# Performance work log

Hardware: AMD Instinct MI355X
Metric: run time of the kernel (lower is better)

Reference implementation:

```python
import jax, jax.numpy as jnp
import numpy as np

N = 1024
H = 128
W = 128
SH_DEG = 3
K = (SH_DEG + 1) ** 2  # 16

C0 = 0.28209479177387814
C1 = 0.4886025119029199
C2 = (1.0925484305920792, -1.0925484305920792, 0.31539156525252005, -1.0925484305920792, 0.5462742152960396)
C3 = (-0.5900435899266435, 2.890611442640554, -0.4570457994644658, 0.3731763325901154, -0.4570457994644658, 1.445305721320277, -0.5900435899266435)


def setup_inputs() -> dict:
    key = jax.random.key(0)
    ks = jax.random.split(key, 8)
    xy = jax.random.uniform(ks[0], (N, 2), minval=-2.0, maxval=2.0)
    z = jax.random.uniform(ks[1], (N, 1), minval=2.0, maxval=8.0)
    means3D = jnp.concatenate([xy, z], axis=1)
    sh = jax.random.normal(ks[2], (N, K, 3)) * 0.3
    opacities = jax.random.uniform(ks[3], (N,), minval=0.1, maxval=1.0)
    scales = jax.random.uniform(ks[4], (N, 3), minval=0.02, maxval=0.15)
    rotations = jax.random.normal(ks[5], (N, 4))
    cam_pos = jnp.zeros((3,), jnp.float32)
    cam_rot = jnp.eye(3, dtype=jnp.float32)  # world-to-camera rotation
    tan_half_fov = jnp.array([0.7], jnp.float32)
    bg_color = jax.random.uniform(ks[6], (3,))
    near_far = jnp.array([0.2, 100.0], jnp.float32)
    return dict(means3D=means3D, sh=sh, opacities=opacities, scales=scales,
                rotations=rotations, cam_pos=cam_pos, cam_rot=cam_rot,
                tan_half_fov=tan_half_fov, bg_color=bg_color, near_far=near_far,
                image_h=H, image_w=W, sh_degree=SH_DEG)


def _eval_sh(sh, dirs):
    # degree-3 real spherical harmonics, as in the 3DGS CUDA rasterizer
    x, y, z = dirs[:, 0:1], dirs[:, 1:2], dirs[:, 2:3]
    res = C0 * sh[:, 0]
    res = res - C1 * y * sh[:, 1] + C1 * z * sh[:, 2] - C1 * x * sh[:, 3]
    xx, yy, zz = x * x, y * y, z * z
    xy, yz, xz = x * y, y * z, x * z
    res = (res + C2[0] * xy * sh[:, 4] + C2[1] * yz * sh[:, 5]
           + C2[2] * (2.0 * zz - xx - yy) * sh[:, 6]
           + C2[3] * xz * sh[:, 7] + C2[4] * (xx - yy) * sh[:, 8])
    res = (res + C3[0] * y * (3.0 * xx - yy) * sh[:, 9]
           + C3[1] * xy * z * sh[:, 10]
           + C3[2] * y * (4.0 * zz - xx - yy) * sh[:, 11]
           + C3[3] * z * (2.0 * zz - 3.0 * xx - 3.0 * yy) * sh[:, 12]
           + C3[4] * x * (4.0 * zz - xx - yy) * sh[:, 13]
           + C3[5] * z * (xx - yy) * sh[:, 14]
           + C3[6] * x * (xx - 3.0 * yy) * sh[:, 15])
    return jnp.maximum(res + 0.5, 0.0)


def _quat_to_rot(q):
    q = q / jnp.linalg.norm(q, axis=1, keepdims=True)
    r, x, y, z = q[:, 0], q[:, 1], q[:, 2], q[:, 3]
    R = jnp.stack([
        1 - 2 * (y * y + z * z), 2 * (x * y - r * z), 2 * (x * z + r * y),
        2 * (x * y + r * z), 1 - 2 * (x * x + z * z), 2 * (y * z - r * x),
        2 * (x * z - r * y), 2 * (y * z + r * x), 1 - 2 * (x * x + y * y)],
        axis=1).reshape(-1, 3, 3)
    return R


def _forward(means3D, sh, opacities, scales, rotations, cam_pos, cam_rot,
             tan_half_fov, bg_color, near_far, image_h, image_w):
    thf = tan_half_fov[0]
    fx = image_w / (2.0 * thf)
    fy = image_h / (2.0 * thf)
    # view-space positions
    t = jnp.einsum('ij,nj->ni', cam_rot, means3D - cam_pos)  # [N,3]
    tz = t[:, 2]
    lim = 1.3 * thf
    tx = jnp.clip(t[:, 0] / tz, -lim, lim) * tz
    ty = jnp.clip(t[:, 1] / tz, -lim, lim) * tz
    # 3D covariance from quaternion + scale: Sigma = (R S)(R S)^T
    Rq = _quat_to_rot(rotations)
    M = Rq * scales[:, None, :]
    cov3 = jnp.einsum('nij,nkj->nik', M, M)
    # EWA splatting: 2D covariance via projection Jacobian
    z2 = tz * tz
    zeros = jnp.zeros_like(tz)
    J = jnp.stack([
        jnp.stack([fx / tz, zeros, -fx * tx / z2], axis=1),
        jnp.stack([zeros, fy / tz, -fy * ty / z2], axis=1)], axis=1)  # [N,2,3]
    T = jnp.einsum('nij,jk->nik', J, cam_rot)
    cov2 = jnp.einsum('nij,njk,nlk->nil', T, cov3, T)  # [N,2,2]
    a = cov2[:, 0, 0] + 0.3  # low-pass filter on diagonal (as in 3DGS)
    c = cov2[:, 1, 1] + 0.3
    b = cov2[:, 0, 1]
    det = a * c - b * b
    inv_det = 1.0 / det
    conA, conB, conC = c * inv_det, -b * inv_det, a * inv_det
    # 2D means in pixel coordinates
    mx = fx * t[:, 0] / tz + (image_w - 1.0) / 2.0
    my = fy * t[:, 1] / tz + (image_h - 1.0) / 2.0
    # view-dependent color from SH
    dirs = means3D - cam_pos
    dirs = dirs / jnp.linalg.norm(dirs, axis=1, keepdims=True)
    colors = _eval_sh(sh, dirs)  # [N,3]
    # per-pixel gaussian alpha [N, P]
    pxs = jnp.arange(image_w, dtype=jnp.float32)
    pys = jnp.arange(image_h, dtype=jnp.float32)
    gy, gx = jnp.meshgrid(pys, pxs, indexing='ij')
    px = gx.reshape(-1)
    py = gy.reshape(-1)
    dx = px[None, :] - mx[:, None]
    dy = py[None, :] - my[:, None]
    power = -0.5 * (conA[:, None] * dx * dx + conC[:, None] * dy * dy) - conB[:, None] * dx * dy
    alpha = jnp.minimum(opacities[:, None] * jnp.exp(power), 0.99)
    valid = (tz > near_far[0]) & (tz < near_far[1]) & (det > 0.0)
    alpha = jnp.where(valid[:, None] & (power <= 0.0) & (alpha >= 1.0 / 255.0), alpha, 0.0)
    # global depth sort + front-to-back alpha compositing
    order = jnp.argsort(tz)
    alpha_s = alpha[order]
    colors_s = colors[order]
    trans = jnp.cumprod(1.0 - alpha_s, axis=0)  # inclusive transmittance [N,P]
    trans_excl = jnp.concatenate([jnp.ones((1, alpha_s.shape[1]), alpha_s.dtype), trans[:-1]], axis=0)
    wgt = alpha_s * trans_excl  # blending weights
    img = jnp.einsum('np,nc->pc', wgt, colors_s) + trans[-1][:, None] * bg_color[None, :]
    return img.reshape(image_h, image_w, 3).transpose(2, 0, 1)  # [3,H,W]


def reference(means3D, sh, opacities, scales, rotations, cam_pos, cam_rot,
              tan_half_fov, bg_color, near_far, image_h, image_w, sh_degree):
    # sh_degree is fixed to 3 via the SH table size (K=16); kept for signature parity
    return _forward(means3D, sh, opacities, scales, rotations, cam_pos, cam_rot,
                    tan_half_fov, bg_color, near_far, image_h, image_w)
```

## Files before the change

### kernel.cpp

```cpp
#include <hip/hip_runtime.h>

#define NG   1024
#define IMH  128
#define IMW  128
#define NPIX (IMH * IMW)
#define SEGS 16

__global__ __launch_bounds__(256) void k_prep(
    const float* __restrict__ means,
    const float* __restrict__ sh,
    const float* __restrict__ opac,
    const float* __restrict__ scales,
    const float* __restrict__ rots,
    const float* __restrict__ campos,
    const float* __restrict__ camrot,
    const float* __restrict__ thf_p,
    const float* __restrict__ nearfar,
    float4* __restrict__ g0, float4* __restrict__ g1, float4* __restrict__ g2)
{
    __shared__ unsigned long long lk[NG];
    __shared__ int prank[16][16];

    int t = threadIdx.x;
    int b = blockIdx.x;

    float thf = thf_p[0];
    float R[9];
    #pragma unroll
    for (int k = 0; k < 9; k++) R[k] = camrot[k];
    float cp0 = campos[0], cp1 = campos[1], cp2 = campos[2];
    float near_ = nearfar[0], far_ = nearfar[1];

    #pragma unroll
    for (int j = 0; j < 4; j++) {
        int g = j * 256 + t;
        float dx = means[3 * g + 0] - cp0;
        float dy = means[3 * g + 1] - cp1;
        float dz = means[3 * g + 2] - cp2;
        float tzk = R[6] * dx + R[7] * dy + R[8] * dz;
        unsigned u = __float_as_uint(tzk);
        u = (u & 0x80000000u) ? ~u : (u | 0x80000000u);
        lk[g] = ((unsigned long long)u << 32) | (unsigned)g;
    }
    __syncthreads();

    int gl    = t & 15;
    int chunk = t >> 4;
    unsigned long long ki = lk[b * 16 + gl];
    int cnt = 0;
    int j0 = chunk * 64;
    #pragma unroll 8
    for (int j = 0; j < 64; j++) cnt += (lk[j0 + j] < ki) ? 1 : 0;
    prank[chunk][gl] = cnt;
    __syncthreads();

    if (t < 16) {
        int i = b * 16 + t;
        float fx = IMW / (2.0f * thf);
        float fy = IMH / (2.0f * thf);

        int r = 0;
        #pragma unroll
        for (int c2i = 0; c2i < 16; c2i++) r += prank[c2i][t];

        float d0x = means[3 * i + 0] - cp0;
        float d0y = means[3 * i + 1] - cp1;
        float d0z = means[3 * i + 2] - cp2;

        float tx0 = R[0] * d0x + R[1] * d0y + R[2] * d0z;
        float ty0 = R[3] * d0x + R[4] * d0y + R[5] * d0z;
        float tz  = R[6] * d0x + R[7] * d0y + R[8] * d0z;

        float lim  = 1.3f * thf;
        float invz = 1.0f / tz;
        float txc  = fminf(fmaxf(tx0 * invz, -lim), lim) * tz;
        float tyc  = fminf(fmaxf(ty0 * invz, -lim), lim) * tz;

        float4 q = ((const float4*)rots)[i];
        float qr = q.x, qx = q.y, qy = q.z, qz = q.w;
        float qn = rsqrtf(qr * qr + qx * qx + qy * qy + qz * qz);
        qr *= qn; qx *= qn; qy *= qn; qz *= qn;
        float Rq0 = 1.0f - 2.0f * (qy * qy + qz * qz);
        float Rq1 = 2.0f * (qx * qy - qr * qz);
        float Rq2 = 2.0f * (qx * qz + qr * qy);
        float Rq3 = 2.0f * (qx * qy + qr * qz);
        float Rq4 = 1.0f - 2.0f * (qx * qx + qz * qz);
        float Rq5 = 2.0f * (qy * qz - qr * qx);
        float Rq6 = 2.0f * (qx * qz - qr * qy);
        float Rq7 = 2.0f * (qy * qz + qr * qx);
        float Rq8 = 1.0f - 2.0f * (qx * qx + qy * qy);

        float sx = scales[3 * i + 0], sy = scales[3 * i + 1], sz = scales[3 * i + 2];
        float M0 = Rq0 * sx, M1 = Rq1 * sy, M2 = Rq2 * sz;
        float M3 = Rq3 * sx, M4 = Rq4 * sy, M5 = Rq5 * sz;
        float M6 = Rq6 * sx, M7 = Rq7 * sy, M8 = Rq8 * sz;

        float c00 = M0 * M0 + M1 * M1 + M2 * M2;
        float c01 = M0 * M3 + M1 * M4 + M2 * M5;
        float c02 = M0 * M6 + M1 * M7 + M2 * M8;
        float c11 = M3 * M3 + M4 * M4 + M5 * M5;
        float c12 = M3 * M6 + M4 * M7 + M5 * M8;
        float c22 = M6 * M6 + M7 * M7 + M8 * M8;

        float z2  = tz * tz;
        float J00 = fx * invz, J02 = -fx * txc / z2;
        float J11 = fy * invz, J12 = -fy * tyc / z2;

        float T00 = J00 * R[0] + J02 * R[6];
        float T01 = J00 * R[1] + J02 * R[7];
        float T02 = J00 * R[2] + J02 * R[8];
        float T10 = J11 * R[3] + J12 * R[6];
        float T11 = J11 * R[4] + J12 * R[7];
        float T12 = J11 * R[5] + J12 * R[8];

        float v00 = T00 * c00 + T01 * c01 + T02 * c02;
        float v01 = T00 * c01 + T01 * c11 + T02 * c12;
        float v02 = T00 * c02 + T01 * c12 + T02 * c22;
        float v10 = T10 * c00 + T11 * c01 + T12 * c02;
        float v11 = T10 * c01 + T11 * c11 + T12 * c12;
        float v12 = T10 * c02 + T11 * c12 + T12 * c22;

        float a  = v00 * T00 + v01 * T01 + v02 * T02 + 0.3f;
        float bb = v00 * T10 + v01 * T11 + v02 * T12;
        float c  = v10 * T10 + v11 * T11 + v12 * T12 + 0.3f;

        float det    = a * c - bb * bb;
        float invdet = 1.0f / det;
        float conA = c * invdet, conB = -bb * invdet, conC = a * invdet;

        float mx = fx * tx0 * invz + (IMW - 1) * 0.5f;
        float my = fy * ty0 * invz + (IMH - 1) * 0.5f;

        float dn = rsqrtf(d0x * d0x + d0y * d0y + d0z * d0z);
        float x = d0x * dn, y = d0y * dn, z = d0z * dn;
        float xx = x * x, yy = y * y, zz = z * z;
        float xy = x * y, yz = y * z, xz = x * z;

        float basis[16];
        basis[0]  = 0.28209479177387814f;
        basis[1]  = -0.4886025119029199f * y;
        basis[2]  =  0.4886025119029199f * z;
        basis[3]  = -0.4886025119029199f * x;
        basis[4]  =  1.0925484305920792f * xy;
        basis[5]  = -1.0925484305920792f * yz;
        basis[6]  =  0.31539156525252005f * (2.0f * zz - xx - yy);
        basis[7]  = -1.0925484305920792f * xz;
        basis[8]  =  0.5462742152960396f * (xx - yy);
        basis[9]  = -0.5900435899266435f * y * (3.0f * xx - yy);
        basis[10] =  2.890611442640554f * xy * z;
        basis[11] = -0.4570457994644658f * y * (4.0f * zz - xx - yy);
        basis[12] =  0.3731763325901154f * z * (2.0f * zz - 3.0f * xx - 3.0f * yy);
        basis[13] = -0.4570457994644658f * x * (4.0f * zz - xx - yy);
        basis[14] =  1.445305721320277f * z * (xx - yy);
        basis[15] = -0.5900435899266435f * x * (xx - 3.0f * yy);

        float f[48];
        {
            const float4* sh4 = (const float4*)(sh + i * 48);
            float4* fv = (float4*)f;
            #pragma unroll
            for (int j = 0; j < 12; j++) fv[j] = sh4[j];
        }
        float colr = 0.0f, colg = 0.0f, colb = 0.0f;
        #pragma unroll
        for (int k = 0; k < 16; k++) {
            float bk = basis[k];
            colr = fmaf(bk, f[3 * k + 0], colr);
            colg = fmaf(bk, f[3 * k + 1], colg);
            colb = fmaf(bk, f[3 * k + 2], colb);
        }
        colr = fmaxf(colr + 0.5f, 0.0f);
        colg = fmaxf(colg + 0.5f, 0.0f);
        colb = fmaxf(colb + 0.5f, 0.0f);

        bool valid = (tz > near_) && (tz < far_) && (det > 0.0f);
        float op = valid ? opac[i] : 0.0f;

        float rx, ry;
        if (op >= (1.0f / 255.0f)) {
            float s2 = 2.0f * logf(255.0f * op);
            rx = sqrtf(s2 * a) + 1e-3f;
            ry = sqrtf(s2 * c) + 1e-3f;
        } else {
            rx = -1.0f; ry = -1.0f;
        }

        g0[r] = make_float4(mx, my, rx, ry);
        g1[r] = make_float4(-0.5f * conA, -conB, -0.5f * conC, op);
        g2[r] = make_float4(colr, colg, colb, 0.0f);
    }
}

__global__ __launch_bounds__(1024) void k_comp(
    const float4* __restrict__ g0, const float4* __restrict__ g1,
    const float4* __restrict__ g2, const float* __restrict__ bg,
    float* __restrict__ out)
{
    __shared__ float4 lA[NG];
    __shared__ float4 lB[NG];
    __shared__ float  lC[NG];
    __shared__ float4 red[SEGS * 64];
    __shared__ int wcnt[16];

    int t    = threadIdx.x;
    int wid  = t >> 6;
    int lane = t & 63;
    int bx = blockIdx.x & 15, by = blockIdx.x >> 4;
    float x0 = (float)(bx * 8), y0 = (float)(by * 8);

    float4 c0 = g0[t];
    float4 c1 = g1[t];
    float4 c2 = g2[t];
    bool surv = (c0.z >= 0.0f) &&
                (c0.x + c0.z >= x0) && (c0.x - c0.z <= x0 + 7.0f) &&
                (c0.y + c0.w >= y0) && (c0.y - c0.w <= y0 + 7.0f);
    unsigned long long m = __ballot(surv);
    if (lane == 0) wcnt[wid] = __popcll(m);
    __syncthreads();

    int pre = 0, M = 0;
    #pragma unroll
    for (int w = 0; w < 16; w++) {
        int cw = wcnt[w];
        M += cw;
        if (w < wid) pre += cw;
    }
    if (surv) {
        int pos = pre + __popcll(m & ((1ull << lane) - 1ull));
        lA[pos] = make_float4(c0.x, c0.y, c1.x, c1.y);
        lB[pos] = make_float4(c1.z, c1.w, c2.x, c2.y);
        lC[pos] = c2.z;
    }
    __syncthreads();

    M = __builtin_amdgcn_readfirstlane(M);
    int len = (M + SEGS - 1) / SEGS;
    int seg = __builtin_amdgcn_readfirstlane(wid);
    int ks  = seg * len;
    int ke  = min(M, ks + len);

    float fpx = x0 + (float)(lane & 7);
    float fpy = y0 + (float)(lane >> 3);

    float T = 1.0f, cr = 0.0f, cg = 0.0f, cb = 0.0f;
    for (int k = ks; k < ke; k++) {
        float4 qA = lA[k];
        float4 qB = lB[k];
        float  qc = lC[k];
        float dx = fpx - qA.x;
        float dy = fpy - qA.y;
        float pw = fmaf(dx, fmaf(qA.z, dx, qA.w * dy), qB.x * (dy * dy));
        float al = qB.y * __expf(pw);
        al = fminf(al, 0.99f);
        bool ok = (pw <= 0.0f) && (al >= (1.0f / 255.0f));
        al = ok ? al : 0.0f;
        float w = al * T;
        cr = fmaf(w, qB.z, cr);
        cg = fmaf(w, qB.w, cg);
        cb = fmaf(w, qc, cb);
        T = fmaf(-al, T, T);
    }

    red[seg * 64 + lane] = make_float4(cr, cg, cb, T);
    __syncthreads();

    if (t < 64) {
        float Tt = 1.0f, r = 0.0f, g = 0.0f, b = 0.0f;
        #pragma unroll
        for (int s = 0; s < SEGS; s++) {
            float4 v = red[s * 64 + t];
            r = fmaf(Tt, v.x, r);
            g = fmaf(Tt, v.y, g);
            b = fmaf(Tt, v.z, b);
            Tt *= v.w;
        }
        int pix = (by * 8 + (t >> 3)) * IMW + bx * 8 + (t & 7);
        out[0 * NPIX + pix] = r + Tt * bg[0];
        out[1 * NPIX + pix] = g + Tt * bg[1];
        out[2 * NPIX + pix] = b + Tt * bg[2];
    }
}

extern "C" void kernel_launch(void* const* d_in, const int* in_sizes, int n_in,
                              void* d_out, int out_size, void* d_ws, size_t ws_size,
                              hipStream_t stream)
{
    (void)in_sizes; (void)n_in; (void)out_size; (void)ws_size;

    const float* means   = (const float*)d_in[0];
    const float* sh      = (const float*)d_in[1];
    const float* opac    = (const float*)d_in[2];
    const float* scales  = (const float*)d_in[3];
    const float* rots    = (const float*)d_in[4];
    const float* campos  = (const float*)d_in[5];
    const float* camrot  = (const float*)d_in[6];
    const float* thf     = (const float*)d_in[7];
    const float* bg      = (const float*)d_in[8];
    const float* nearfar = (const float*)d_in[9];

    char* ws = (char*)d_ws;
    float4* g0 = (float4*)(ws + 0);
    float4* g1 = (float4*)(ws + 16384);
    float4* g2 = (float4*)(ws + 32768);

    k_prep<<<64, 256, 0, stream>>>(means, sh, opac, scales, rots, campos,
                                   camrot, thf, nearfar, g0, g1, g2);
    k_comp<<<256, 1024, 0, stream>>>(g0, g1, g2, bg, (float*)d_out);
}
```

Before: 85.53 us.

## Fuse preprocessing into compositing kernel with per-tile culling and local depth sort

```diff
diff --git a/kernel.cpp b/kernel.cpp
--- a/kernel.cpp
+++ b/kernel.cpp
@@ -6,7 +6,7 @@
 #define NPIX (IMH * IMW)
 #define SEGS 16
 
-__global__ __launch_bounds__(256) void k_prep(
+__global__ __launch_bounds__(1024) void k_fused(
     const float* __restrict__ means,
     const float* __restrict__ sh,
     const float* __restrict__ opac,
@@ -16,123 +16,147 @@
     const float* __restrict__ camrot,
     const float* __restrict__ thf_p,
     const float* __restrict__ nearfar,
-    float4* __restrict__ g0, float4* __restrict__ g1, float4* __restrict__ g2)
+    const float* __restrict__ bg,
+    float* __restrict__ out)
 {
-    __shared__ unsigned long long lk[NG];
-    __shared__ int prank[16][16];
-
-    int t = threadIdx.x;
-    int b = blockIdx.x;
+    __shared__ float4 uA[NG];
+    __shared__ float2 uB[NG];
+    __shared__ unsigned long long ukey[NG];
+    __shared__ float4 lA[NG];
+    __shared__ float4 lB[NG];
+    __shared__ float  lC[NG];
+    __shared__ float4 red[SEGS * 64];
+    __shared__ int wcnt[16];
+
+    int t    = threadIdx.x;
+    int wid  = t >> 6;
+    int lane = t & 63;
+    int bx = blockIdx.x & 15, by = blockIdx.x >> 4;
+    float x0 = (float)(bx * 8), y0 = (float)(by * 8);
 
     float thf = thf_p[0];
+    float fx = IMW / (2.0f * thf);
+    float fy = IMH / (2.0f * thf);
     float R[9];
     #pragma unroll
     for (int k = 0; k < 9; k++) R[k] = camrot[k];
     float cp0 = campos[0], cp1 = campos[1], cp2 = campos[2];
     float near_ = nearfar[0], far_ = nearfar[1];
 
+    float d0x = means[3 * t + 0] - cp0;
+    float d0y = means[3 * t + 1] - cp1;
+    float d0z = means[3 * t + 2] - cp2;
+
+    float tx0 = R[0] * d0x + R[1] * d0y + R[2] * d0z;
+    float ty0 = R[3] * d0x + R[4] * d0y + R[5] * d0z;
+    float tz  = R[6] * d0x + R[7] * d0y + R[8] * d0z;
+
+    float lim  = 1.3f * thf;
+    float invz = 1.0f / tz;
+    float txc  = fminf(fmaxf(tx0 * invz, -lim), lim) * tz;
+    float tyc  = fminf(fmaxf(ty0 * invz, -lim), lim) * tz;
+
+    float4 q = ((const float4*)rots)[t];
+    float qr = q.x, qx = q.y, qy = q.z, qz = q.w;
+    float qn = rsqrtf(qr * qr + qx * qx + qy * qy + qz * qz);
+    qr *= qn; qx *= qn; qy *= qn; qz *= qn;
+    float Rq0 = 1.0f - 2.0f * (qy * qy + qz * qz);
+    float Rq1 = 2.0f * (qx * qy - qr * qz);
+    float Rq2 = 2.0f * (qx * qz + qr * qy);
+    float Rq3 = 2.0f * (qx * qy + qr * qz);
+    float Rq4 = 1.0f - 2.0f * (qx * qx + qz * qz);
+    float Rq5 = 2.0f * (qy * qz - qr * qx);
+    float Rq6 = 2.0f * (qx * qz - qr * qy);
+    float Rq7 = 2.0f * (qy * qz + qr * qx);
+    float Rq8 = 1.0f - 2.0f * (qx * qx + qy * qy);
+
+    float sx = scales[3 * t + 0], sy = scales[3 * t + 1], sz = scales[3 * t + 2];
+    float M0 = Rq0 * sx, M1 = Rq1 * sy, M2 = Rq2 * sz;
+    float M3 = Rq3 * sx, M4 = Rq4 * sy, M5 = Rq5 * sz;
+    float M6 = Rq6 * sx, M7 = Rq7 * sy, M8 = Rq8 * sz;
+
+    float c00 = M0 * M0 + M1 * M1 + M2 * M2;
+    float c01 = M0 * M3 + M1 * M4 + M2 * M5;
+    float c02 = M0 * M6 + M1 * M7 + M2 * M8;
+    float c11 = M3 * M3 + M4 * M4 + M5 * M5;
+    float c12 = M3 * M6 + M4 * M7 + M5 * M8;
+    float c22 = M6 * M6 + M7 * M7 + M8 * M8;
+
+    float z2  = tz * tz;
+    float J00 = fx * invz, J02 = -fx * txc / z2;
+    float J11 = fy * invz, J12 = -fy * tyc / z2;
+
+    float T00 = J00 * R[0] + J02 * R[6];
+    float T01 = J00 * R[1] + J02 * R[7];
+    float T02 = J00 * R[2] + J02 * R[8];
+    float T10 = J11 * R[3] + J12 * R[6];
+    float T11 = J11 * R[4] + J12 * R[7];
+    float T12 = J11 * R[5] + J12 * R[8];
+
+    float v00 = T00 * c00 + T01 * c01 + T02 * c02;
+    float v01 = T00 * c01 + T01 * c11 + T02 * c12;
+    float v02 = T00 * c02 + T01 * c12 + T02 * c22;
+    float v10 = T10 * c00 + T11 * c01 + T12 * c02;
+    float v11 = T10 * c01 + T11 * c11 + T12 * c12;
+    float v12 = T10 * c02 + T11 * c12 + T12 * c22;
+
+    float a  = v00 * T00 + v01 * T01 + v02 * T02 + 0.3f;
+    float bb = v00 * T10 + v01 * T11 + v02 * T12;
+    float c  = v10 * T10 + v11 * T11 + v12 * T12 + 0.3f;
+
+    float det    = a * c - bb * bb;
+    float invdet = 1.0f / det;
+    float conA = c * invdet, conB = -bb * invdet, conC = a * invdet;
+
+    float mx = fx * tx0 * invz + (IMW - 1) * 0.5f;
+    float my = fy * ty0 * invz + (IMH - 1) * 0.5f;
+
+    bool valid = (tz > near_) && (tz < far_) && (det > 0.0f);
+    float op = valid ? opac[t] : 0.0f;
+
+    float rx = -1.0f, ry = -1.0f;
+    if (op >= (1.0f / 255.0f)) {
+        float s2 = 2.0f * logf(255.0f * op);
+        rx = sqrtf(s2 * a) + 1e-3f;
+        ry = sqrtf(s2 * c) + 1e-3f;
+    }
+
+    bool surv = (rx >= 0.0f) &&
+                (mx + rx >= x0) && (mx - rx <= x0 + 7.0f) &&
+                (my + ry >= y0) && (my - ry <= y0 + 7.0f);
+    unsigned long long m = __ballot(surv);
+    if (lane == 0) wcnt[wid] = __popcll(m);
+    __syncthreads();
+
+    int pre = 0, M = 0;
     #pragma unroll
-    for (int j = 0; j < 4; j++) {
-        int g = j * 256 + t;
-        float dx = means[3 * g + 0] - cp0;
-        float dy = means[3 * g + 1] - cp1;
-        float dz = means[3 * g + 2] - cp2;
-        float tzk = R[6] * dx + R[7] * dy + R[8] * dz;
-        unsigned u = __float_as_uint(tzk);
+    for (int w = 0; w < 16; w++) {
+        int cw = wcnt[w];
+        M += cw;
+        if (w < wid) pre += cw;
+    }
+    if (surv) {
+        int pos = pre + __popcll(m & ((1ull << lane) - 1ull));
+        uA[pos] = make_float4(mx, my, -0.5f * conA, -conB);
+        uB[pos] = make_float2(-0.5f * conC, op);
+        unsigned u = __float_as_uint(tz);
         u = (u & 0x80000000u) ? ~u : (u | 0x80000000u);
-        lk[g] = ((unsigned long long)u << 32) | (unsigned)g;
-    }
-    __syncthreads();
-
-    int gl    = t & 15;
-    int chunk = t >> 4;
-    unsigned long long ki = lk[b * 16 + gl];
-    int cnt = 0;
-    int j0 = chunk * 64;
-    #pragma unroll 8
-    for (int j = 0; j < 64; j++) cnt += (lk[j0 + j] < ki) ? 1 : 0;
-    prank[chunk][gl] = cnt;
-    __syncthreads();
-
-    if (t < 16) {
-        int i = b * 16 + t;
-        float fx = IMW / (2.0f * thf);
-        float fy = IMH / (2.0f * thf);
-
+        ukey[pos] = ((unsigned long long)u << 32) | (unsigned)t;
+    }
+    __syncthreads();
+
+    if (t < M) {
+        unsigned long long kt = ukey[t];
         int r = 0;
-        #pragma unroll
-        for (int c2i = 0; c2i < 16; c2i++) r += prank[c2i][t];
-
-        float d0x = means[3 * i + 0] - cp0;
-        float d0y = means[3 * i + 1] - cp1;
-        float d0z = means[3 * i + 2] - cp2;
-
-        float tx0 = R[0] * d0x + R[1] * d0y + R[2] * d0z;
-        float ty0 = R[3] * d0x + R[4] * d0y + R[5] * d0z;
-        float tz  = R[6] * d0x + R[7] * d0y + R[8] * d0z;
-
-        float lim  = 1.3f * thf;
-        float invz = 1.0f / tz;
-        float txc  = fminf(fmaxf(tx0 * invz, -lim), lim) * tz;
-        float tyc  = fminf(fmaxf(ty0 * invz, -lim), lim) * tz;
-
-        float4 q = ((const float4*)rots)[i];
-        float qr = q.x, qx = q.y, qy = q.z, qz = q.w;
-        float qn = rsqrtf(qr * qr + qx * qx + qy * qy + qz * qz);
-        qr *= qn; qx *= qn; qy *= qn; qz *= qn;
-        float Rq0 = 1.0f - 2.0f * (qy * qy + qz * qz);
-        float Rq1 = 2.0f * (qx * qy - qr * qz);
-        float Rq2 = 2.0f * (qx * qz + qr * qy);
-        float Rq3 = 2.0f * (qx * qy + qr * qz);
-        float Rq4 = 1.0f - 2.0f * (qx * qx + qz * qz);
-        float Rq5 = 2.0f * (qy * qz - qr * qx);
-        float Rq6 = 2.0f * (qx * qz - qr * qy);
-        float Rq7 = 2.0f * (qy * qz + qr * qx);
-        float Rq8 = 1.0f - 2.0f * (qx * qx + qy * qy);
-
-        float sx = scales[3 * i + 0], sy = scales[3 * i + 1], sz = scales[3 * i + 2];
-        float M0 = Rq0 * sx, M1 = Rq1 * sy, M2 = Rq2 * sz;
-        float M3 = Rq3 * sx, M4 = Rq4 * sy, M5 = Rq5 * sz;
-        float M6 = Rq6 * sx, M7 = Rq7 * sy, M8 = Rq8 * sz;
-
-        float c00 = M0 * M0 + M1 * M1 + M2 * M2;
-        float c01 = M0 * M3 + M1 * M4 + M2 * M5;
-        float c02 = M0 * M6 + M1 * M7 + M2 * M8;
-        float c11 = M3 * M3 + M4 * M4 + M5 * M5;
-        float c12 = M3 * M6 + M4 * M7 + M5 * M8;
-        float c22 = M6 * M6 + M7 * M7 + M8 * M8;
-
-        float z2  = tz * tz;
-        float J00 = fx * invz, J02 = -fx * txc / z2;
-        float J11 = fy * invz, J12 = -fy * tyc / z2;
-
-        float T00 = J00 * R[0] + J02 * R[6];
-        float T01 = J00 * R[1] + J02 * R[7];
-        float T02 = J00 * R[2] + J02 * R[8];
-        float T10 = J11 * R[3] + J12 * R[6];
-        float T11 = J11 * R[4] + J12 * R[7];
-        float T12 = J11 * R[5] + J12 * R[8];
-
-        float v00 = T00 * c00 + T01 * c01 + T02 * c02;
-        float v01 = T00 * c01 + T01 * c11 + T02 * c12;
-        float v02 = T00 * c02 + T01 * c12 + T02 * c22;
-        float v10 = T10 * c00 + T11 * c01 + T12 * c02;
-        float v11 = T10 * c01 + T11 * c11 + T12 * c12;
-        float v12 = T10 * c02 + T11 * c12 + T12 * c22;
-
-        float a  = v00 * T00 + v01 * T01 + v02 * T02 + 0.3f;
-        float bb = v00 * T10 + v01 * T11 + v02 * T12;
-        float c  = v10 * T10 + v11 * T11 + v12 * T12 + 0.3f;
-
-        float det    = a * c - bb * bb;
-        float invdet = 1.0f / det;
-        float conA = c * invdet, conB = -bb * invdet, conC = a * invdet;
-
-        float mx = fx * tx0 * invz + (IMW - 1) * 0.5f;
-        float my = fy * ty0 * invz + (IMH - 1) * 0.5f;
-
-        float dn = rsqrtf(d0x * d0x + d0y * d0y + d0z * d0z);
-        float x = d0x * dn, y = d0y * dn, z = d0z * dn;
+        for (int j = 0; j < M; j++) r += (ukey[j] < kt) ? 1 : 0;
+
+        int idx = (int)(kt & 0xffffffffu);
+
+        float gx = means[3 * idx + 0] - cp0;
+        float gy = means[3 * idx + 1] - cp1;
+        float gz = means[3 * idx + 2] - cp2;
+        float dn = rsqrtf(gx * gx + gy * gy + gz * gz);
+        float x = gx * dn, y = gy * dn, z = gz * dn;
         float xx = x * x, yy = y * y, zz = z * z;
         float xy = x * y, yz = y * z, xz = x * z;
 
@@ -156,7 +180,7 @@
 
         float f[48];
         {
-            const float4* sh4 = (const float4*)(sh + i * 48);
+            const float4* sh4 = (const float4*)(sh + idx * 48);
             float4* fv = (float4*)f;
             #pragma unroll
             for (int j = 0; j < 12; j++) fv[j] = sh4[j];
@@ -173,67 +197,14 @@
         colg = fmaxf(colg + 0.5f, 0.0f);
         colb = fmaxf(colb + 0.5f, 0.0f);
 
-        bool valid = (tz > near_) && (tz < far_) && (det > 0.0f);
-        float op = valid ? opac[i] : 0.0f;
-
-        float rx, ry;
-        if (op >= (1.0f / 255.0f)) {
-            float s2 = 2.0f * logf(255.0f * op);
-            rx = sqrtf(s2 * a) + 1e-3f;
-            ry = sqrtf(s2 * c) + 1e-3f;
-        } else {
-            rx = -1.0f; ry = -1.0f;
-        }
-
-        g0[r] = make_float4(mx, my, rx, ry);
-        g1[r] = make_float4(-0.5f * conA, -conB, -0.5f * conC, op);
-        g2[r] = make_float4(colr, colg, colb, 0.0f);
-    }
-}
-
-__global__ __launch_bounds__(1024) void k_comp(
-    const float4* __restrict__ g0, const float4* __restrict__ g1,
-    const float4* __restrict__ g2, const float* __restrict__ bg,
-    float* __restrict__ out)
-{
-    __shared__ float4 lA[NG];
-    __shared__ float4 lB[NG];
-    __shared__ float  lC[NG];
-    __shared__ float4 red[SEGS * 64];
-    __shared__ int wcnt[16];
-
-    int t    = threadIdx.x;
-    int wid  = t >> 6;
-    int lane = t & 63;
-    int bx = blockIdx.x & 15, by = blockIdx.x >> 4;
-    float x0 = (float)(bx * 8), y0 = (float)(by * 8);
-
-    float4 c0 = g0[t];
-    float4 c1 = g1[t];
-    float4 c2 = g2[t];
-    bool surv = (c0.z >= 0.0f) &&
-                (c0.x + c0.z >= x0) && (c0.x - c0.z <= x0 + 7.0f) &&
-                (c0.y + c0.w >= y0) && (c0.y - c0.w <= y0 + 7.0f);
-    unsigned long long m = __ballot(surv);
-    if (lane == 0) wcnt[wid] = __popcll(m);
-    __syncthreads();
-
-    int pre = 0, M = 0;
-    #pragma unroll
-    for (int w = 0; w < 16; w++) {
-        int cw = wcnt[w];
-        M += cw;
-        if (w < wid) pre += cw;
-    }
-    if (surv) {
-        int pos = pre + __popcll(m & ((1ull << lane) - 1ull));
-        lA[pos] = make_float4(c0.x, c0.y, c1.x, c1.y);
-        lB[pos] = make_float4(c1.z, c1.w, c2.x, c2.y);
-        lC[pos] = c2.z;
-    }
-    __syncthreads();
-
-    M = __builtin_amdgcn_readfirstlane(M);
+        float4 ua = uA[t];
+        float2 ub = uB[t];
+        lA[r] = ua;
+        lB[r] = make_float4(ub.x, ub.y, colr, colg);
+        lC[r] = colb;
+    }
+    __syncthreads();
+
     int len = (M + SEGS - 1) / SEGS;
     int seg = __builtin_amdgcn_readfirstlane(wid);
     int ks  = seg * len;
@@ -285,7 +256,7 @@
                               void* d_out, int out_size, void* d_ws, size_t ws_size,
                               hipStream_t stream)
 {
-    (void)in_sizes; (void)n_in; (void)out_size; (void)ws_size;
+    (void)in_sizes; (void)n_in; (void)out_size; (void)d_ws; (void)ws_size;
 
     const float* means   = (const float*)d_in[0];
     const float* sh      = (const float*)d_in[1];
@@ -298,12 +269,6 @@
     const float* bg      = (const float*)d_in[8];
     const float* nearfar = (const float*)d_in[9];
 
-    char* ws = (char*)d_ws;
-    float4* g0 = (float4*)(ws + 0);
-    float4* g1 = (float4*)(ws + 16384);
-    float4* g2 = (float4*)(ws + 32768);
-
-    k_prep<<<64, 256, 0, stream>>>(means, sh, opac, scales, rots, campos,
-                                   camrot, thf, nearfar, g0, g1, g2);
-    k_comp<<<256, 1024, 0, stream>>>(g0, g1, g2, bg, (float*)d_out);
+    k_fused<<<256, 1024, 0, stream>>>(means, sh, opac, scales, rots, campos,
+                                      camrot, thf, nearfar, bg, (float*)d_out);
 }
```

Result: faster. 83.75 us (-2.1%).
